# Kernel optimization log

Hardware: AMD Instinct MI355X
Metric: run time of the kernel (lower is better)

The kernel has to match this reference:

```python
import jax, jax.numpy as jnp
import numpy as np

EPS = 1e-5  # torch InstanceNorm2d default eps

def conv1x1(x, w, b):
    # x: [B,C,H,W], w: [O,C], b: [O]
    return jnp.einsum('bchw,oc->bohw', x, w) + b[None, :, None, None]

def instance_norm(x):
    # InstanceNorm2d(affine=False): normalize per-sample, per-channel over H,W
    mean = jnp.mean(x, axis=(2, 3), keepdims=True)
    var = jnp.var(x, axis=(2, 3), keepdims=True)
    return (x - mean) * jax.lax.rsqrt(var + EPS)

def proj(x, w, b):
    return jax.nn.relu(instance_norm(conv1x1(x, w, b)))

def setup_inputs() -> dict:
    key = jax.random.key(0)
    ks = jax.random.split(key, 9)
    B, C, Ci, H, W = 16, 256, 128, 64, 64
    s_in = 1.0 / np.sqrt(C)
    s_mid = 1.0 / np.sqrt(Ci)
    return {
        'x': jax.random.normal(ks[0], (B, C, H, W), jnp.float32),
        'g_w': jax.random.normal(ks[1], (Ci, C), jnp.float32) * s_in,
        'g_b': jax.random.normal(ks[2], (Ci,), jnp.float32) * s_in,
        'theta_w': jax.random.normal(ks[3], (Ci, C), jnp.float32) * s_in,
        'theta_b': jax.random.normal(ks[4], (Ci,), jnp.float32) * s_in,
        'phi_w': jax.random.normal(ks[5], (Ci, C), jnp.float32) * s_in,
        'phi_b': jax.random.normal(ks[6], (Ci,), jnp.float32) * s_in,
        'W_w': jax.random.normal(ks[7], (C, Ci), jnp.float32) * s_mid,
        'W_b': jax.random.normal(ks[8], (C,), jnp.float32) * s_mid,
    }

def reference(x, g_w, g_b, theta_w, theta_b, phi_w, phi_b, W_w, W_b):
    B, C, H, W = x.shape
    Ci = g_w.shape[0]
    N = H * W
    g_x = proj(x, g_w, g_b).reshape(B, Ci, N)        # [B,Ci,N]
    theta_x = proj(x, theta_w, theta_b).reshape(B, Ci, N)
    phi_x = proj(x, phi_w, phi_b).reshape(B, Ci, N)
    # channel-attention Gram matrix [B,Ci,Ci], softmax over last dim
    f = jnp.einsum('bin,bjn->bij', theta_x, phi_x)
    attn = jax.nn.softmax(f, axis=2)
    y = jnp.einsum('bij,bjn->bin', attn, g_x)        # [B,Ci,N]
    # replicate torch permute(0,2,1).contiguous().view(B,Ci,H,W)
    y = jnp.transpose(y, (0, 2, 1)).reshape(B, Ci, H, W)
    y = instance_norm(conv1x1(y, W_w, W_b))
    return y + x
```

## Files before the change

### kernel.cpp

```cpp
#include <hip/hip_runtime.h>

#define DEVINL __device__ __forceinline__

typedef __attribute__((ext_vector_type(8))) _Float16 h8v;
typedef __attribute__((ext_vector_type(4))) float f32x4;
typedef __attribute__((ext_vector_type(8))) unsigned short us8;
typedef __attribute__((ext_vector_type(4))) unsigned short us4;

DEVINL unsigned short f2h(float f) {
  return __builtin_bit_cast(unsigned short, (_Float16)f);
}
DEVINL float h2f(unsigned short u) {
  return (float)__builtin_bit_cast(_Float16, u);
}

__global__ __launch_bounds__(512, 2)
void proj_gemm(const unsigned short* __restrict__ wall_h,
               const unsigned short* __restrict__ wall_l,
               const float* __restrict__ x,
               unsigned short* __restrict__ zh, unsigned short* __restrict__ zl,
               float* __restrict__ partials)
{
  __shared__ __align__(16) unsigned short As_h[384 * 72];
  __shared__ __align__(16) unsigned short As_l[256 * 72];
  __shared__ __align__(16) unsigned short Bs_h[128 * 72];
  __shared__ __align__(16) unsigned short Bs_l[128 * 72];

  const int t = threadIdx.x;
  const int lane = t & 63;
  const int wave = t >> 6;
  const int wm = wave >> 1, wn = wave & 1;
  const int lr = lane & 15, lk = lane >> 4;
  const int b = blockIdx.z;
  const int bx = blockIdx.x;
  const int nbase = bx * 128;
  const float* xs = x + (long)b * 256 * 4096;

  f32x4 acc[6][4];
#pragma unroll
  for (int i = 0; i < 6; ++i)
#pragma unroll
    for (int j = 0; j < 4; ++j) acc[i][j] = (f32x4)0.0f;

  const int nl = t & 127, cg = t >> 7;

  for (int kt = 0; kt < 4; ++kt) {
    const int k0 = kt * 64;
#pragma unroll
    for (int i = 0; i < 6; ++i) {
      const int q = i * 512 + t;
      const int row = q >> 3, c = q & 7;
      *(us8*)&As_h[row * 72 + c * 8] = *(const us8*)&wall_h[(long)row * 256 + k0 + c * 8];
    }
#pragma unroll
    for (int i = 0; i < 4; ++i) {
      const int q = i * 512 + t;
      const int row = q >> 3, c = q & 7;
      *(us8*)&As_l[row * 72 + c * 8] = *(const us8*)&wall_l[(long)row * 256 + k0 + c * 8];
    }
#pragma unroll
    for (int hp = 0; hp < 2; ++hp) {
      float xv[8];
#pragma unroll
      for (int i = 0; i < 8; ++i)
        xv[i] = xs[(long)(k0 + cg * 16 + hp * 8 + i) * 4096 + nbase + nl];
      us8 h8, l8;
#pragma unroll
      for (int e = 0; e < 8; ++e) {
        const unsigned short hb = f2h(xv[e]);
        h8[e] = hb;
        l8[e] = f2h(xv[e] - h2f(hb));
      }
      *(us8*)&Bs_h[nl * 72 + cg * 16 + hp * 8] = h8;
      *(us8*)&Bs_l[nl * 72 + cg * 16 + hp * 8] = l8;
    }
    __syncthreads();

#pragma unroll
    for (int ks = 0; ks < 2; ++ks) {
      const int ko = ks * 32 + lk * 8;
      h8v bh[4], bl[4];
#pragma unroll
      for (int ni = 0; ni < 4; ++ni) {
        const int r = (wn * 64 + ni * 16 + lr) * 72 + ko;
        bh[ni] = *(const h8v*)&Bs_h[r];
        bl[ni] = *(const h8v*)&Bs_l[r];
      }
#pragma unroll
      for (int mi = 0; mi < 6; ++mi) {
        const int fr = mi * 4 + wm;
        const h8v ah = *(const h8v*)&As_h[(fr * 16 + lr) * 72 + ko];
        if (fr < 16) {
          const h8v al = *(const h8v*)&As_l[(fr * 16 + lr) * 72 + ko];
#pragma unroll
          for (int ni = 0; ni < 4; ++ni) {
            acc[mi][ni] = __builtin_amdgcn_mfma_f32_16x16x32_f16(bh[ni], ah, acc[mi][ni], 0, 0, 0);
            acc[mi][ni] = __builtin_amdgcn_mfma_f32_16x16x32_f16(bl[ni], ah, acc[mi][ni], 0, 0, 0);
            acc[mi][ni] = __builtin_amdgcn_mfma_f32_16x16x32_f16(bh[ni], al, acc[mi][ni], 0, 0, 0);
          }
        } else {
#pragma unroll
          for (int ni = 0; ni < 4; ++ni)
            acc[mi][ni] = __builtin_amdgcn_mfma_f32_16x16x32_f16(bh[ni], ah, acc[mi][ni], 0, 0, 0);
        }
      }
    }
    __syncthreads();
  }

  float* sbuf = (float*)As_h;
#pragma unroll
  for (int mi = 0; mi < 6; ++mi) {
    float s = 0.f, ss = 0.f;
#pragma unroll
    for (int ni = 0; ni < 4; ++ni)
#pragma unroll
      for (int r = 0; r < 4; ++r) {
        const float v = acc[mi][ni][r];
        s += v; ss += v * v;
      }
    const int fr = mi * 4 + wm;
    const int slot = ((fr * 16 + lr) * 8 + (wn * 4 + lk)) * 2;
    sbuf[slot] = s; sbuf[slot + 1] = ss;
  }
  __syncthreads();
  if (t < 384) {
    float s = 0.f, ss = 0.f;
#pragma unroll
    for (int w = 0; w < 8; ++w) {
      s += sbuf[(t * 8 + w) * 2];
      ss += sbuf[(t * 8 + w) * 2 + 1];
    }
    const long pidx = ((long)bx * 6144 + b * 384 + t) * 2;
    partials[pidx] = s; partials[pidx + 1] = ss;
  }

#pragma unroll
  for (int mi = 0; mi < 6; ++mi)
#pragma unroll
    for (int ni = 0; ni < 4; ++ni) {
      const int gm = (mi * 4 + wm) * 16 + lr;
      const int gn = nbase + wn * 64 + ni * 16 + lk * 4;
      us4 hv, lv;
#pragma unroll
      for (int r = 0; r < 4; ++r) {
        const float v = acc[mi][ni][r];
        const unsigned short h = f2h(v);
        hv[r] = h;
        lv[r] = f2h(v - h2f(h));
      }
      *(us4*)&zh[((long)b * 384 + gm) * 4096 + gn] = hv;
      if (gm < 256) *(us4*)&zl[((long)b * 256 + gm) * 4096 + gn] = lv;
    }
}

__global__ __launch_bounds__(256)
void stats_reduce(const float* __restrict__ partials, float* __restrict__ stats)
{
  const int row = blockIdx.x * 256 + threadIdx.x;
  float s = 0.f, ss = 0.f;
#pragma unroll
  for (int k = 0; k < 32; ++k) {
    s += partials[((long)k * 6144 + row) * 2];
    ss += partials[((long)k * 6144 + row) * 2 + 1];
  }
  const float mean = s * (1.f / 4096.f);
  const float var = ss * (1.f / 4096.f) - mean * mean;
  const float rs = rsqrtf(fmaxf(var, 0.f) + 1e-5f);
  stats[row * 2] = rs;
  stats[row * 2 + 1] = -mean * rs;
}

__global__ __launch_bounds__(256, 2)
void fgemm_norm(const unsigned short* __restrict__ zh, const unsigned short* __restrict__ zl,
                const float* __restrict__ stats, float* __restrict__ fpart)
{
  __shared__ __align__(16) unsigned short As_h[128 * 72];
  __shared__ __align__(16) unsigned short As_l[128 * 72];
  __shared__ __align__(16) unsigned short Bs_h[128 * 72];
  __shared__ __align__(16) unsigned short Bs_l[128 * 72];

  const int t = threadIdx.x;
  const int lane = t & 63;
  const int wave = t >> 6;
  const int wm = wave >> 1, wn = wave & 1;
  const int lr = lane & 15, lk = lane >> 4;
  const int zb = blockIdx.z >> 5, z1 = blockIdx.z & 31;
  const int koff = z1 * 128;

  f32x4 acc[4][4];
#pragma unroll
  for (int i = 0; i < 4; ++i)
#pragma unroll
    for (int j = 0; j < 4; ++j) acc[i][j] = (f32x4)0.0f;

  for (int kt = 0; kt < 2; ++kt) {
    const int k0 = koff + kt * 64;
#pragma unroll
    for (int i = 0; i < 4; ++i) {
      const int q = i * 256 + t;
      const int row = q >> 3, c = q & 7;
#pragma unroll
      for (int op = 0; op < 2; ++op) {
        const int zrow = op * 128 + row;
        const us8 h = *(const us8*)&zh[((long)zb * 384 + zrow) * 4096 + k0 + c * 8];
        const us8 l = *(const us8*)&zl[((long)zb * 256 + zrow) * 4096 + k0 + c * 8];
        const int srow = zb * 384 + zrow;
        const float rs = stats[srow * 2];
        const float nmrs = stats[srow * 2 + 1];
        us8 oh, ol;
#pragma unroll
        for (int e = 0; e < 8; ++e) {
          const float v = h2f(h[e]) + h2f(l[e]);
          const float nv = fmaxf(__builtin_fmaf(v, rs, nmrs), 0.f);
          const unsigned short hb = f2h(nv);
          oh[e] = hb;
          ol[e] = f2h(nv - h2f(hb));
        }
        unsigned short* dh = op ? Bs_h : As_h;
        unsigned short* dl = op ? Bs_l : As_l;
        *(us8*)&dh[row * 72 + c * 8] = oh;
        *(us8*)&dl[row * 72 + c * 8] = ol;
      }
    }
    __syncthreads();
#pragma unroll
    for (int ks = 0; ks < 2; ++ks) {
      const int ko = ks * 32 + lk * 8;
      h8v ah[4], bh[4], al[4], bl[4];
#pragma unroll
      for (int mi = 0; mi < 4; ++mi) {
        const int r = (wm * 64 + mi * 16 + lr) * 72 + ko;
        ah[mi] = *(const h8v*)&As_h[r];
        al[mi] = *(const h8v*)&As_l[r];
      }
#pragma unroll
      for (int ni = 0; ni < 4; ++ni) {
        const int r = (wn * 64 + ni * 16 + lr) * 72 + ko;
        bh[ni] = *(const h8v*)&Bs_h[r];
        bl[ni] = *(const h8v*)&Bs_l[r];
      }
#pragma unroll
      for (int mi = 0; mi < 4; ++mi)
#pragma unroll
        for (int ni = 0; ni < 4; ++ni) {
          acc[mi][ni] = __builtin_amdgcn_mfma_f32_16x16x32_f16(bh[ni], ah[mi], acc[mi][ni], 0, 0, 0);
          acc[mi][ni] = __builtin_amdgcn_mfma_f32_16x16x32_f16(bl[ni], ah[mi], acc[mi][ni], 0, 0, 0);
          acc[mi][ni] = __builtin_amdgcn_mfma_f32_16x16x32_f16(bh[ni], al[mi], acc[mi][ni], 0, 0, 0);
        }
    }
    __syncthreads();
  }

  const long cOff = ((long)zb * 32 + z1) * 16384;
#pragma unroll
  for (int mi = 0; mi < 4; ++mi)
#pragma unroll
    for (int ni = 0; ni < 4; ++ni) {
      const int gm = wm * 64 + mi * 16 + lr;
      const int gn = wn * 64 + ni * 16 + lk * 4;
      *(f32x4*)&fpart[cOff + (long)gm * 128 + gn] = acc[mi][ni];
    }
}

__global__ __launch_bounds__(256, 2)
void gemm_y(const unsigned short* __restrict__ Ah0, const unsigned short* __restrict__ Bh0,
            unsigned short* __restrict__ Cout,
            int lda, int ldb, int ldc, int ksteps, int z1count,
            long aS1, long aS2, long bS1, long bS2, long cS1, long cS2)
{
  __shared__ __align__(16) unsigned short As[128 * 72];
  __shared__ __align__(16) unsigned short Bs[128 * 72];

  const int t = threadIdx.x;
  const int lane = t & 63;
  const int wave = t >> 6;
  const int wm = wave >> 1, wn = wave & 1;
  const int lr = lane & 15, lk = lane >> 4;

  const int z = blockIdx.z;
  const int zb = z / z1count, z1 = z - zb * z1count;
  const unsigned short* Ah = Ah0 + zb * aS2 + z1 * aS1;
  const unsigned short* Bh = Bh0 + zb * bS2 + z1 * bS1;
  const long cOff = zb * cS2 + z1 * cS1;

  f32x4 acc[4][4];
#pragma unroll
  for (int i = 0; i < 4; ++i)
#pragma unroll
    for (int j = 0; j < 4; ++j) acc[i][j] = (f32x4)0.0f;

  for (int kt = 0; kt < ksteps; ++kt) {
    const int k0 = kt * 64;
#pragma unroll
    for (int i = 0; i < 4; ++i) {
      const int q = i * 256 + t;
      const int row = q >> 3, c = q & 7;
      const int lo = row * 72 + c * 8;
      *(us8*)&As[lo] = *(const us8*)&Ah[(long)row * lda + k0 + c * 8];
      *(us8*)&Bs[lo] = *(const us8*)&Bh[(long)row * ldb + k0 + c * 8];
    }
    __syncthreads();
#pragma unroll
    for (int ks = 0; ks < 2; ++ks) {
      const int ko = ks * 32 + lk * 8;
      h8v ah[4], bh[4];
#pragma unroll
      for (int mi = 0; mi < 4; ++mi)
        ah[mi] = *(const h8v*)&As[(wm * 64 + mi * 16 + lr) * 72 + ko];
#pragma unroll
      for (int ni = 0; ni < 4; ++ni)
        bh[ni] = *(const h8v*)&Bs[(wn * 64 + ni * 16 + lr) * 72 + ko];
#pragma unroll
      for (int mi = 0; mi < 4; ++mi)
#pragma unroll
        for (int ni = 0; ni < 4; ++ni)
          acc[mi][ni] = __builtin_amdgcn_mfma_f32_16x16x32_f16(bh[ni], ah[mi], acc[mi][ni], 0, 0, 0);
    }
    __syncthreads();
  }

#pragma unroll
  for (int mi = 0; mi < 4; ++mi)
#pragma unroll
    for (int ni = 0; ni < 4; ++ni) {
      const int gm = wm * 64 + mi * 16 + lr;
      const int gn = wn * 64 + ni * 16 + lk * 4;
      const f32x4 v = acc[mi][ni];
      us4 o;
#pragma unroll
      for (int r = 0; r < 4; ++r) o[r] = f2h(v[r]);
      *(us4*)&Cout[cOff + (long)gm * ldc + gn] = o;
    }
}

__global__ __launch_bounds__(256, 2)
void conv2_gemm(const unsigned short* __restrict__ w2h,
                const unsigned short* __restrict__ y4T,
                unsigned short* __restrict__ z2b)
{
  __shared__ __align__(16) unsigned short As[256 * 72];
  __shared__ __align__(16) unsigned short Bs[128 * 72];

  const int t = threadIdx.x;
  const int lane = t & 63;
  const int wave = t >> 6;
  const int wm = wave >> 1, wn = wave & 1;
  const int lr = lane & 15, lk = lane >> 4;
  const int b = blockIdx.z;
  const int nbase = blockIdx.x * 128;
  const unsigned short* Bh = y4T + (long)b * 4096 * 128 + (long)nbase * 128;

  f32x4 acc[8][4];
#pragma unroll
  for (int i = 0; i < 8; ++i)
#pragma unroll
    for (int j = 0; j < 4; ++j) acc[i][j] = (f32x4)0.0f;

  for (int kt = 0; kt < 2; ++kt) {
    const int k0 = kt * 64;
#pragma unroll
    for (int i = 0; i < 8; ++i) {
      const int q = i * 256 + t;
      const int row = q >> 3, c = q & 7;
      *(us8*)&As[row * 72 + c * 8] = *(const us8*)&w2h[(long)row * 128 + k0 + c * 8];
    }
#pragma unroll
    for (int i = 0; i < 4; ++i) {
      const int q = i * 256 + t;
      const int row = q >> 3, c = q & 7;
      *(us8*)&Bs[row * 72 + c * 8] = *(const us8*)&Bh[(long)row * 128 + k0 + c * 8];
    }
    __syncthreads();
#pragma unroll
    for (int ks = 0; ks < 2; ++ks) {
      const int ko = ks * 32 + lk * 8;
      h8v ah[8], bh[4];
#pragma unroll
      for (int mi = 0; mi < 8; ++mi)
        ah[mi] = *(const h8v*)&As[(wm * 128 + mi * 16 + lr) * 72 + ko];
#pragma unroll
      for (int ni = 0; ni < 4; ++ni)
        bh[ni] = *(const h8v*)&Bs[(wn * 64 + ni * 16 + lr) * 72 + ko];
#pragma unroll
      for (int mi = 0; mi < 8; ++mi)
#pragma unroll
        for (int ni = 0; ni < 4; ++ni)
          acc[mi][ni] = __builtin_amdgcn_mfma_f32_16x16x32_f16(bh[ni], ah[mi], acc[mi][ni], 0, 0, 0);
    }
    __syncthreads();
  }

#pragma unroll
  for (int mi = 0; mi < 8; ++mi)
#pragma unroll
    for (int ni = 0; ni < 4; ++ni) {
      const int gm = wm * 128 + mi * 16 + lr;
      const int gn = nbase + wn * 64 + ni * 16 + lk * 4;
      const f32x4 v = acc[mi][ni];
      us4 o;
#pragma unroll
      for (int r = 0; r < 4; ++r) o[r] = f2h(v[r]);
      *(us4*)&z2b[((long)b * 256 + gm) * 4096 + gn] = o;
    }
}

__global__ __launch_bounds__(256)
void prep_weights(const float* __restrict__ g_w, const float* __restrict__ th_w,
                  const float* __restrict__ ph_w, const float* __restrict__ W_w,
                  unsigned short* __restrict__ wall_h, unsigned short* __restrict__ wall_l,
                  unsigned short* __restrict__ w2h)
{
  const int i = blockIdx.x * 256 + threadIdx.x;
  float v;
  if (i < 32768) v = th_w[i];
  else if (i < 65536) v = ph_w[i - 32768];
  else v = g_w[i - 65536];
  const unsigned short h = f2h(v);
  wall_h[i] = h;
  if (i < 65536) wall_l[i] = f2h(v - h2f(h));
  if (i < 32768) w2h[i] = f2h(W_w[i]);
}

__global__ __launch_bounds__(256)
void norm_transpose_g(const unsigned short* __restrict__ zh,
                      const float* __restrict__ stats,
                      unsigned short* __restrict__ gT)
{
  __shared__ unsigned short T[64 * 136];
  const int b = blockIdx.y, n0 = blockIdx.x * 64;
  const int t = threadIdx.x;
  const int c = t >> 1, part = t & 1;
  const int grow = b * 384 + 256 + c;
  const float rs = stats[grow * 2];
  const float nmrs = stats[grow * 2 + 1];
  const long off = (long)grow * 4096 + n0 + part * 32;
#pragma unroll
  for (int j = 0; j < 4; ++j) {
    const us8 h = *(const us8*)&zh[off + j * 8];
#pragma unroll
    for (int e = 0; e < 8; ++e) {
      const float nv = fmaxf(__builtin_fmaf(h2f(h[e]), rs, nmrs), 0.f);
      T[(part * 32 + j * 8 + e) * 136 + c] = f2h(nv);
    }
  }
  __syncthreads();
  const int nl = t >> 2, q = t & 3;
  const long obase = ((long)b * 4096 + n0 + nl) * 128 + q * 32;
#pragma unroll
  for (int k = 0; k < 4; ++k) {
    us8 o;
#pragma unroll
    for (int e = 0; e < 8; ++e) o[e] = T[nl * 136 + q * 32 + k * 8 + e];
    *(us8*)&gT[obase + k * 8] = o;
  }
}

__global__ __launch_bounds__(64)
void softmax_attn(const float* __restrict__ fpart, unsigned short* __restrict__ attn)
{
  const int row = blockIdx.x;
  const int b = row >> 7, i = row & 127;
  const int t = threadIdx.x;
  float v0 = 0.f, v1 = 0.f;
#pragma unroll
  for (int kc = 0; kc < 32; ++kc) {
    const float* p = fpart + ((long)(b * 32 + kc)) * 16384 + i * 128;
    v0 += p[t];
    v1 += p[t + 64];
  }
  float mx = fmaxf(v0, v1);
  for (int o = 32; o > 0; o >>= 1) mx = fmaxf(mx, __shfl_xor(mx, o));
  const float e0 = __expf(v0 - mx), e1 = __expf(v1 - mx);
  float s = e0 + e1;
  for (int o = 32; o > 0; o >>= 1) s += __shfl_xor(s, o);
  const float inv = 1.f / s;
  attn[(long)row * 128 + t] = f2h(e0 * inv);
  attn[(long)row * 128 + t + 64] = f2h(e1 * inv);
}

__global__ __launch_bounds__(256)
void finalize(const unsigned short* __restrict__ z2b, const float* __restrict__ x,
              float* __restrict__ out)
{
  const int row = blockIdx.x;
  const long base = (long)row * 4096;
  const int t = threadIdx.x;
  float v[16];
  float s = 0.f, ss = 0.f;
#pragma unroll
  for (int h = 0; h < 2; ++h) {
    us8 u = *(const us8*)&z2b[base + t * 16 + h * 8];
#pragma unroll
    for (int e = 0; e < 8; ++e) {
      const float f = h2f(u[e]);
      v[h * 8 + e] = f;
      s += f; ss += f * f;
    }
  }
  __shared__ float r0[256], r1[256];
  r0[t] = s; r1[t] = ss;
  __syncthreads();
  for (int o = 128; o > 0; o >>= 1) {
    if (t < o) { r0[t] += r0[t + o]; r1[t] += r1[t + o]; }
    __syncthreads();
  }
  const float mean = r0[0] * (1.f / 4096.f);
  const float var = r1[0] * (1.f / 4096.f) - mean * mean;
  const float rs = rsqrtf(fmaxf(var, 0.f) + 1e-5f);
#pragma unroll
  for (int i = 0; i < 4; ++i) {
    f32x4 xr = *(const f32x4*)&x[base + t * 16 + i * 4];
    f32x4 o;
#pragma unroll
    for (int e = 0; e < 4; ++e) o[e] = (v[i * 4 + e] - mean) * rs + xr[e];
    *(f32x4*)&out[base + t * 16 + i * 4] = o;
  }
}

extern "C" void kernel_launch(void* const* d_in, const int* in_sizes, int n_in,
                              void* d_out, int out_size, void* d_ws, size_t ws_size,
                              hipStream_t stream)
{
  const float* x    = (const float*)d_in[0];
  const float* g_w  = (const float*)d_in[1];
  const float* th_w = (const float*)d_in[3];
  const float* ph_w = (const float*)d_in[5];
  const float* W_w  = (const float*)d_in[7];

  char* ws = (char*)d_ws;
  const size_t MB = 1024ull * 1024ull;
  if (ws_size < 186 * MB) return;

  unsigned short* zh       = (unsigned short*)(ws);
  unsigned short* zl       = (unsigned short*)(ws + 51 * MB);
  float*          fpart    = (float*)(ws + 85 * MB);
  unsigned short* attn     = (unsigned short*)(ws + 119 * MB);
  unsigned short* gT       = (unsigned short*)(ws + 120 * MB);
  unsigned short* y4T      = (unsigned short*)(ws + 137 * MB);
  unsigned short* z2b      = (unsigned short*)(ws);
  float*          partials = (float*)(ws + 154 * MB);
  float*          stats    = (float*)(ws + 158 * MB);
  unsigned short* wall_h   = (unsigned short*)(ws + 159 * MB);
  unsigned short* wall_l   = (unsigned short*)(ws + 159 * MB + 256 * 1024);
  unsigned short* w2h      = (unsigned short*)(ws + 159 * MB + 512 * 1024);

  prep_weights<<<dim3(384), 256, 0, stream>>>(g_w, th_w, ph_w, W_w, wall_h, wall_l, w2h);

  proj_gemm<<<dim3(32, 1, 16), 512, 0, stream>>>(wall_h, wall_l, x, zh, zl, partials);

  stats_reduce<<<dim3(24), 256, 0, stream>>>(partials, stats);

  norm_transpose_g<<<dim3(64, 16), 256, 0, stream>>>(zh, stats, gT);

  fgemm_norm<<<dim3(1, 1, 512), 256, 0, stream>>>(zh, zl, stats, fpart);

  softmax_attn<<<dim3(2048), 64, 0, stream>>>(fpart, attn);

  gemm_y<<<dim3(1, 1, 512), 256, 0, stream>>>(
      attn, gT, y4T,
      128, 4096, 128, 2, 32,
      0, 16384, 128, (long)4096 * 128, 16384, (long)4096 * 128);

  conv2_gemm<<<dim3(32, 1, 16), 256, 0, stream>>>(w2h, y4T, z2b);

  finalize<<<dim3(4096), 256, 0, stream>>>(z2b, x, (float*)d_out);
}
```

Before: 162.0 us.

## Pre-swizzle projection weights into MFMA fragment order and read them from global

prep_weights now writes the fp16 hi/lo projection weights in a fragment-major layout matching the MFMA A-operand access pattern. proj_gemm reads these fragments straight from global memory (L2-cached) instead of staging them through LDS, which cuts LDS use to the B tiles only and raises the launch-bounds occupancy hint. This removes the per-k-tile weight staging stores and LDS pressure, at the cost of more global/L2 load traffic inside the MFMA loop that may add latency.

Measured after the change: 332.0 us. 2.05x slower.

```diff
diff --git a/kernel.cpp b/kernel.cpp
--- a/kernel.cpp
+++ b/kernel.cpp
@@ -14,17 +14,41 @@
   return (float)__builtin_bit_cast(_Float16, u);
 }
 
-__global__ __launch_bounds__(512, 2)
-void proj_gemm(const unsigned short* __restrict__ wall_h,
-               const unsigned short* __restrict__ wall_l,
+__global__ __launch_bounds__(256)
+void prep_weights(const float* __restrict__ g_w, const float* __restrict__ th_w,
+                  const float* __restrict__ ph_w, const float* __restrict__ W_w,
+                  unsigned short* __restrict__ wallf, unsigned short* __restrict__ wallf_l,
+                  unsigned short* __restrict__ w2h)
+{
+  const int o = blockIdx.x * 256 + threadIdx.x;
+  const int fr = o >> 12;
+  const int rem = o & 4095;
+  const int ko8 = rem >> 7;
+  const int lr = (rem >> 3) & 15;
+  const int e = rem & 7;
+  const int row = fr * 16 + lr;
+  const int col = ko8 * 8 + e;
+  const int i = row * 256 + col;
+  float v;
+  if (row < 128) v = th_w[i];
+  else if (row < 256) v = ph_w[i - 32768];
+  else v = g_w[i - 65536];
+  const unsigned short h = f2h(v);
+  wallf[o] = h;
+  if (row < 256) wallf_l[o] = f2h(v - h2f(h));
+  if (o < 32768) w2h[o] = f2h(W_w[o]);
+}
+
+__global__ __launch_bounds__(512, 4)
+void proj_gemm(const unsigned short* __restrict__ wallf,
+               const unsigned short* __restrict__ wallf_l,
                const float* __restrict__ x,
                unsigned short* __restrict__ zh, unsigned short* __restrict__ zl,
                float* __restrict__ partials)
 {
-  __shared__ __align__(16) unsigned short As_h[384 * 72];
-  __shared__ __align__(16) unsigned short As_l[256 * 72];
-  __shared__ __align__(16) unsigned short Bs_h[128 * 72];
-  __shared__ __align__(16) unsigned short Bs_l[128 * 72];
+  __shared__ __align__(16) unsigned short smem[2 * 128 * 72];
+  unsigned short* Bs_h = smem;
+  unsigned short* Bs_l = smem + 128 * 72;
 
   const int t = threadIdx.x;
   const int lane = t & 63;
@@ -36,6 +60,15 @@
   const int nbase = bx * 128;
   const float* xs = x + (long)b * 256 * 4096;
 
+  const unsigned short* aH[6];
+  const unsigned short* aL[4];
+#pragma unroll
+  for (int mi = 0; mi < 6; ++mi) {
+    const int fr = mi * 4 + wm;
+    aH[mi] = wallf + ((long)fr * 32 * 16 + lr) * 8;
+    if (mi < 4) aL[mi] = wallf_l + ((long)fr * 32 * 16 + lr) * 8;
+  }
+
   f32x4 acc[6][4];
 #pragma unroll
   for (int i = 0; i < 6; ++i)
@@ -46,18 +79,6 @@
 
   for (int kt = 0; kt < 4; ++kt) {
     const int k0 = kt * 64;
-#pragma unroll
-    for (int i = 0; i < 6; ++i) {
-      const int q = i * 512 + t;
-      const int row = q >> 3, c = q & 7;
-      *(us8*)&As_h[row * 72 + c * 8] = *(const us8*)&wall_h[(long)row * 256 + k0 + c * 8];
-    }
-#pragma unroll
-    for (int i = 0; i < 4; ++i) {
-      const int q = i * 512 + t;
-      const int row = q >> 3, c = q & 7;
-      *(us8*)&As_l[row * 72 + c * 8] = *(const us8*)&wall_l[(long)row * 256 + k0 + c * 8];
-    }
 #pragma unroll
     for (int hp = 0; hp < 2; ++hp) {
       float xv[8];
@@ -79,6 +100,7 @@
 #pragma unroll
     for (int ks = 0; ks < 2; ++ks) {
       const int ko = ks * 32 + lk * 8;
+      const int ko8 = (k0 >> 3) + ks * 4 + lk;
       h8v bh[4], bl[4];
 #pragma unroll
       for (int ni = 0; ni < 4; ++ni) {
@@ -88,10 +110,9 @@
       }
 #pragma unroll
       for (int mi = 0; mi < 6; ++mi) {
-        const int fr = mi * 4 + wm;
-        const h8v ah = *(const h8v*)&As_h[(fr * 16 + lr) * 72 + ko];
-        if (fr < 16) {
-          const h8v al = *(const h8v*)&As_l[(fr * 16 + lr) * 72 + ko];
+        const h8v ah = *(const h8v*)&aH[mi][(long)ko8 * 16 * 8];
+        if (mi < 4) {
+          const h8v al = *(const h8v*)&aL[mi][(long)ko8 * 16 * 8];
 #pragma unroll
           for (int ni = 0; ni < 4; ++ni) {
             acc[mi][ni] = __builtin_amdgcn_mfma_f32_16x16x32_f16(bh[ni], ah, acc[mi][ni], 0, 0, 0);
@@ -108,7 +129,7 @@
     __syncthreads();
   }
 
-  float* sbuf = (float*)As_h;
+  float* sbuf = (float*)smem;
 #pragma unroll
   for (int mi = 0; mi < 6; ++mi) {
     float s = 0.f, ss = 0.f;
@@ -406,23 +427,6 @@
 }
 
 __global__ __launch_bounds__(256)
-void prep_weights(const float* __restrict__ g_w, const float* __restrict__ th_w,
-                  const float* __restrict__ ph_w, const float* __restrict__ W_w,
-                  unsigned short* __restrict__ wall_h, unsigned short* __restrict__ wall_l,
-                  unsigned short* __restrict__ w2h)
-{
-  const int i = blockIdx.x * 256 + threadIdx.x;
-  float v;
-  if (i < 32768) v = th_w[i];
-  else if (i < 65536) v = ph_w[i - 32768];
-  else v = g_w[i - 65536];
-  const unsigned short h = f2h(v);
-  wall_h[i] = h;
-  if (i < 65536) wall_l[i] = f2h(v - h2f(h));
-  if (i < 32768) w2h[i] = f2h(W_w[i]);
-}
-
-__global__ __launch_bounds__(256)
 void norm_transpose_g(const unsigned short* __restrict__ zh,
                       const float* __restrict__ stats,
                       unsigned short* __restrict__ gT)
@@ -541,13 +545,13 @@
   unsigned short* z2b      = (unsigned short*)(ws);
   float*          partials = (float*)(ws + 154 * MB);
   float*          stats    = (float*)(ws + 158 * MB);
-  unsigned short* wall_h   = (unsigned short*)(ws + 159 * MB);
-  unsigned short* wall_l   = (unsigned short*)(ws + 159 * MB + 256 * 1024);
+  unsigned short* wallf    = (unsigned short*)(ws + 159 * MB);
+  unsigned short* wallf_l  = (unsigned short*)(ws + 159 * MB + 256 * 1024);
   unsigned short* w2h      = (unsigned short*)(ws + 159 * MB + 512 * 1024);
 
-  prep_weights<<<dim3(384), 256, 0, stream>>>(g_w, th_w, ph_w, W_w, wall_h, wall_l, w2h);
-
-  proj_gemm<<<dim3(32, 1, 16), 512, 0, stream>>>(wall_h, wall_l, x, zh, zl, partials);
+  prep_weights<<<dim3(384), 256, 0, stream>>>(g_w, th_w, ph_w, W_w, wallf, wallf_l, w2h);
+
+  proj_gemm<<<dim3(32, 1, 16), 512, 0, stream>>>(wallf, wallf_l, x, zh, zl, partials);
 
   stats_reduce<<<dim3(24), 256, 0, stream>>>(partials, stats);
 
```
